# Kernel optimization log

Measured on AMD Instinct MI355X. Metric: run time of the kernel, lower is better.

Reference implementation:

```python
import jax, jax.numpy as jnp
import numpy as np

N_NODES = 50000
N_EDGES = 300000
INPUT_DIM = 128
HIDDEN_DIM = 256
NUM_HEADS = 8
HEAD_DIM = HIDDEN_DIM // NUM_HEADS  # 32
NUM_EDGE_TYPES = 3


def setup_inputs() -> dict:
    key = jax.random.key(0)
    ks = jax.random.split(key, 12)
    s_in = 1.0 / np.sqrt(INPUT_DIM)
    s_hid = 1.0 / np.sqrt(HIDDEN_DIM)
    return {
        "node_features": jax.random.normal(ks[0], (N_NODES, INPUT_DIM), jnp.float32),
        "edges": jax.random.randint(ks[1], (N_EDGES, 2), 0, N_NODES),
        "edge_types": jax.random.randint(ks[2], (N_EDGES,), 0, NUM_EDGE_TYPES),
        # torch.nn.Linear convention: y = x @ W.T + b, W: [out, in]
        "Wq": jax.random.normal(ks[3], (HIDDEN_DIM, INPUT_DIM), jnp.float32) * s_in,
        "bq": jax.random.normal(ks[4], (HIDDEN_DIM,), jnp.float32) * s_in,
        "Wk": jax.random.normal(ks[5], (HIDDEN_DIM, INPUT_DIM), jnp.float32) * s_in,
        "bk": jax.random.normal(ks[6], (HIDDEN_DIM,), jnp.float32) * s_in,
        "Wv": jax.random.normal(ks[7], (HIDDEN_DIM, INPUT_DIM), jnp.float32) * s_in,
        "bv": jax.random.normal(ks[8], (HIDDEN_DIM,), jnp.float32) * s_in,
        "edge_emb": jax.random.normal(ks[9], (NUM_EDGE_TYPES, HIDDEN_DIM), jnp.float32),
        "Wo": jax.random.normal(ks[10], (INPUT_DIM, HIDDEN_DIM), jnp.float32) * s_hid,
        "bo": jax.random.normal(ks[11], (INPUT_DIM,), jnp.float32) * s_hid,
    }


def reference(node_features, edges, edge_types, Wq, bq, Wk, bk, Wv, bv, edge_emb, Wo, bo):
    # Project all nodes once, split heads: [N, H, D]
    Q = (node_features @ Wq.T + bq).reshape(-1, NUM_HEADS, HEAD_DIM)
    K = (node_features @ Wk.T + bk).reshape(-1, NUM_HEADS, HEAD_DIM)
    V = (node_features @ Wv.T + bv).reshape(-1, NUM_HEADS, HEAD_DIM)

    src = edges[:, 0]
    tgt = edges[:, 1]

    # Per-edge small attention: Q[src] [E,H,D] x K[tgt]^T -> [E,H,H]
    # (identical math to the original per-edge-type loop, since only the
    #  edge embedding depends on edge_type and it is gathered per edge)
    scale = 1.0 / jnp.sqrt(jnp.float32(HEAD_DIM))
    scores = jnp.einsum("ehd,egd->ehg", Q[src], K[tgt]) * scale
    attn = jax.nn.softmax(scores, axis=-1)
    msg = jnp.einsum("ehg,egd->ehd", attn, V[tgt]).reshape(-1, HIDDEN_DIM)  # [E, HID]

    msg = msg + edge_emb[edge_types]          # per-edge-type embedding add
    out_e = msg @ Wo.T + bo                   # output projection per edge [E, IN]

    # Scatter-add over source nodes (original Python loop over edges)
    messages = jax.ops.segment_sum(out_e, src, num_segments=N_NODES)
    return messages
```

## Files before the change

kernel.cpp:

```cpp
#include <hip/hip_runtime.h>

#define N_NODES 50000
#define N_EDGES 300000
#define M_PAD 50048
#define M_PAD2 50176
#define NBLK 196

typedef __attribute__((ext_vector_type(8))) short bf16x8;
typedef __attribute__((ext_vector_type(4))) short bf16x4;
typedef __attribute__((ext_vector_type(4))) float f32x4;

__device__ __forceinline__ float bf2f(unsigned short h) { return __uint_as_float(((unsigned int)h) << 16); }
__device__ __forceinline__ unsigned short f2bf(float x) {
    unsigned int u = __float_as_uint(x);
    unsigned int r = (u + 0x7FFFu + ((u >> 16) & 1u)) >> 16;
    return (unsigned short)r;
}

template <int MODE>
__global__ __launch_bounds__(MODE == 0 ? 512 : 128)
void mfma_gemm(const unsigned short* __restrict__ A2, const unsigned short* __restrict__ B2,
               const float* __restrict__ biasCat,
               unsigned short* __restrict__ Qb, unsigned short* __restrict__ Kb,
               unsigned short* __restrict__ Vb,
               const float* __restrict__ eew, const float* __restrict__ bo,
               const float4* __restrict__ cnt4, float* __restrict__ Cout)
{
    constexpr int K2  = (MODE == 0) ? 128 : 256;
    constexpr int NWN = (MODE == 0) ? 4 : 2;
    constexpr int BM  = (MODE == 0) ? 128 : 64;
    const int t    = threadIdx.x;
    const int w    = t >> 6;
    const int lane = t & 63;
    const int l15  = lane & 15;
    const int lg   = lane >> 4;
    const int bx   = blockIdx.x;
    const int m0   = blockIdx.y * BM;
    const int n0   = bx * (NWN * 64);
    const int wm   = (w / NWN) * 64;
    const int wn   = (w % NWN) * 64;

    f32x4 acc[4][4] = {};

    const unsigned short* Abase = A2 + (size_t)(m0 + wm + l15) * K2 + lg * 8;
    const unsigned short* Bbase = B2 + (size_t)(n0 + wn + l15) * K2 + lg * 8;

    #pragma unroll 2
    for (int ks = 0; ks < K2 / 32; ++ks) {
        bf16x8 af[4], bfv[4];
        #pragma unroll
        for (int mi = 0; mi < 4; ++mi)
            af[mi] = *(const bf16x8*)(Abase + (size_t)mi * 16 * K2 + ks * 32);
        #pragma unroll
        for (int ni = 0; ni < 4; ++ni)
            bfv[ni] = *(const bf16x8*)(Bbase + (size_t)ni * 16 * K2 + ks * 32);
        #pragma unroll
        for (int mi = 0; mi < 4; ++mi)
            #pragma unroll
            for (int ni = 0; ni < 4; ++ni)
                acc[mi][ni] = __builtin_amdgcn_mfma_f32_16x16x32_bf16(
                    af[mi], bfv[ni], acc[mi][ni], 0, 0, 0);
    }

    if constexpr (MODE == 0) {
        __shared__ unsigned short Cs[64 * 256];
        float bvn[4];
        #pragma unroll
        for (int ni = 0; ni < 4; ++ni)
            bvn[ni] = biasCat[n0 + wn + ni * 16 + l15];

        #pragma unroll
        for (int p = 0; p < 2; ++p) {
            if (p) __syncthreads();
            #pragma unroll
            for (int mi2 = 0; mi2 < 2; ++mi2) {
                const int mi = p * 2 + mi2;
                #pragma unroll
                for (int j = 0; j < 4; ++j) {
                    const int lr = (wm >> 1) + mi2 * 16 + lg * 4 + j;
                    const int xr = (lr & 7) << 3;
                    #pragma unroll
                    for (int ni = 0; ni < 4; ++ni) {
                        const int col = wn + ni * 16 + l15;
                        Cs[lr * 256 + (col ^ xr)] = f2bf(acc[mi][ni][j] + bvn[ni]);
                    }
                }
            }
            __syncthreads();

            if (bx < 2) {
                unsigned short* dst = bx ? Kb : Qb;
                #pragma unroll
                for (int c8 = 0; c8 < 4; ++c8) {
                    const int chunk = c8 * 512 + t;
                    const int lr = chunk >> 5;
                    const int ec = (chunk & 31) * 8;
                    const int gr = m0 + ((lr < 32) ? (p * 32 + lr)
                                                   : (64 + p * 32 + (lr - 32)));
                    const bf16x8 v = *(const bf16x8*)&Cs[lr * 256 + (ec ^ ((lr & 7) << 3))];
                    *(bf16x8*)&dst[(size_t)gr * 256 + ec] = v;
                }
            } else {
                #pragma unroll
                for (int c8 = 0; c8 < 4; ++c8) {
                    const int chunk = c8 * 512 + t;
                    const int lr = chunk >> 5;
                    const int ec = (chunk & 31) * 8;
                    const int gr = m0 + ((lr < 32) ? (p * 32 + lr)
                                                   : (64 + p * 32 + (lr - 32)));
                    const int d  = ec >> 3;
                    const int xr = (lr & 7) << 3;
                    bf16x8 v;
                    #pragma unroll
                    for (int g = 0; g < 8; ++g)
                        v[g] = (short)Cs[lr * 256 + ((g * 32 + d) ^ xr)];
                    *(bf16x8*)&Vb[(size_t)gr * 256 + ec] = v;
                }
            }
        }
    } else {
        #pragma unroll
        for (int mi = 0; mi < 4; ++mi)
            #pragma unroll
            for (int j = 0; j < 4; ++j) {
                const int row = m0 + wm + mi * 16 + lg * 4 + j;
                if (row < N_NODES) {
                    const float4 cv = cnt4[row];
                    #pragma unroll
                    for (int ni = 0; ni < 4; ++ni) {
                        const int col = wn + ni * 16 + l15;
                        Cout[(size_t)row * 128 + col] = acc[mi][ni][j]
                            + cv.x * eew[col] + cv.y * eew[128 + col]
                            + cv.z * eew[256 + col] + cv.w * bo[col];
                    }
                }
            }
    }
}

__global__ __launch_bounds__(256)
void conv_nf_kernel(const float4* __restrict__ nf4, unsigned short* __restrict__ A2)
{
    const int tid = blockIdx.x * 256 + threadIdx.x;
    if (tid >= N_NODES * 32) return;
    const int m = tid >> 5, k4 = (tid & 31) * 4;
    const float4 v = nf4[tid];
    ushort4 hi;
    hi.x = f2bf(v.x); hi.y = f2bf(v.y); hi.z = f2bf(v.z); hi.w = f2bf(v.w);
    *reinterpret_cast<ushort4*>(&A2[(size_t)m * 128 + k4]) = hi;
}

__global__ __launch_bounds__(256)
void prep_kernel(const float* __restrict__ Wq, const float* __restrict__ Wk,
                 const float* __restrict__ Wv, const float* __restrict__ bq,
                 const float* __restrict__ bk, const float* __restrict__ bv,
                 const float* __restrict__ Wo, const float* __restrict__ ee,
                 unsigned short* __restrict__ B2qkv, unsigned short* __restrict__ B2o,
                 float* __restrict__ biasCat, float* __restrict__ eew)
{
    const int bid = blockIdx.x, t = threadIdx.x;
    if (bid < 384) {
        const int tid = bid * 256 + t;
        const int r = tid >> 7, k = tid & 127;
        const float* W = (r < 256) ? Wq : (r < 512) ? Wk : Wv;
        B2qkv[(size_t)r * 128 + k] = f2bf(W[(size_t)(r & 255) * 128 + k]);
        if (k == 0) {
            const float* b = (r < 256) ? bq : (r < 512) ? bk : bv;
            biasCat[r] = b[r & 255];
        }
    } else if (bid < 512) {
        const int tid = (bid - 384) * 256 + t;
        const int r = tid >> 8, k = tid & 255;
        B2o[(size_t)r * 256 + k] = f2bf(Wo[(size_t)r * 256 + k]);
    } else if (t < 128) {
        float a0 = 0.f, a1 = 0.f, a2 = 0.f;
        for (int k = 0; k < 256; ++k) {
            const float w = Wo[(size_t)t * 256 + k];
            a0 += ee[k] * w; a1 += ee[256 + k] * w; a2 += ee[512 + k] * w;
        }
        eew[t] = a0; eew[128 + t] = a1; eew[256 + t] = a2;
    }
}

__global__ __launch_bounds__(256)
void hist_kernel(const int* __restrict__ edges, int* __restrict__ deg)
{
    const int e = blockIdx.x * 256 + threadIdx.x;
    if (e < N_EDGES) atomicAdd(&deg[edges[2 * e]], 1);
}

__global__ __launch_bounds__(256)
void scan_part1(const int* __restrict__ deg, int* __restrict__ blockSum)
{
    const int t = threadIdx.x;
    const int i = blockIdx.x * 256 + t;
    int v = (i < N_NODES) ? deg[i] : 0;
    #pragma unroll
    for (int o = 1; o < 64; o <<= 1) v += __shfl_xor(v, o);
    __shared__ int ws[4];
    if ((t & 63) == 0) ws[t >> 6] = v;
    __syncthreads();
    if (t == 0) blockSum[blockIdx.x] = ws[0] + ws[1] + ws[2] + ws[3];
}

__global__ __launch_bounds__(256)
void scan_part2(const int* __restrict__ blockSum, int* __restrict__ blockBase,
                int* __restrict__ rowStart)
{
    __shared__ int lds[256];
    const int t = threadIdx.x;
    lds[t] = (t < NBLK) ? blockSum[t] : 0;
    __syncthreads();
    #pragma unroll
    for (int o = 1; o < 256; o <<= 1) {
        const int u = (t >= o) ? lds[t - o] : 0;
        __syncthreads();
        lds[t] += u;
        __syncthreads();
    }
    if (t < NBLK) blockBase[t] = (t == 0) ? 0 : lds[t - 1];
    if (t == 0) rowStart[N_NODES] = N_EDGES;
}

__global__ __launch_bounds__(256)
void scan_part3(const int* __restrict__ deg, const int* __restrict__ blockBase,
                int* __restrict__ rowStart, int* __restrict__ cursor)
{
    const int t = threadIdx.x;
    const int lane = t & 63, wid = t >> 6;
    const int i = blockIdx.x * 256 + t;
    const int d = (i < N_NODES) ? deg[i] : 0;
    int x = d;
    #pragma unroll
    for (int o = 1; o < 64; o <<= 1) {
        const int u = __shfl_up(x, o);
        if (lane >= o) x += u;
    }
    __shared__ int wtot[4];
    if (lane == 63) wtot[wid] = x;
    __syncthreads();
    int wo = 0;
    #pragma unroll
    for (int wi = 0; wi < 3; ++wi) wo += (wi < wid) ? wtot[wi] : 0;
    const int excl = blockBase[blockIdx.x] + wo + x - d;
    if (i < N_NODES) { rowStart[i] = excl; cursor[i] = excl; }
}

__global__ __launch_bounds__(256)
void scatter_kernel(const int* __restrict__ edges, const int* __restrict__ etypes,
                    int* __restrict__ cursor, int* __restrict__ packed)
{
    const int e = blockIdx.x * 256 + threadIdx.x;
    if (e < N_EDGES) {
        const int pos = atomicAdd(&cursor[edges[2 * e]], 1);
        packed[pos] = edges[2 * e + 1] | (etypes[e] << 20);
    }
}

__global__ __launch_bounds__(256)
void node_gather_kernel(const int* __restrict__ packed, const int* __restrict__ rowStart,
                        const unsigned short* __restrict__ Qb,
                        const unsigned short* __restrict__ Kb,
                        const unsigned short* __restrict__ Vb,
                        unsigned short* __restrict__ accQ, float4* __restrict__ cnt4)
{
    const int lane = threadIdx.x & 63;
    const int n = blockIdx.x * 4 + (threadIdx.x >> 6);
    if (n >= N_NODES) return;
    const int l15 = lane & 15;
    const int lg  = lane >> 4;

    const bf16x8 qf = *(const bf16x8*)&Qb[(size_t)n * 256 + (l15 & 7) * 32 + lg * 8];

    f32x4 cpv0 = {0.f, 0.f, 0.f, 0.f};
    f32x4 cpv1 = {0.f, 0.f, 0.f, 0.f};
    int c0 = 0, c1 = 0, c2 = 0;

    const int lo = rowStart[n], hi = rowStart[n + 1];
    const bool validBase = ((l15 < 8) == (lg < 2));

    for (int idx = lo; idx < hi; idx += 2) {
        const int  p0  = packed[idx];
        const bool dup = (idx + 1 >= hi);
        const int  p1  = dup ? p0 : packed[idx + 1];
        const int  t0  = p0 & 0xFFFFF;
        const int  t1  = p1 & 0xFFFFF;
        const int  e0  = p0 >> 20;
        const int  e1  = p1 >> 20;
        c0 += (e0 == 0); c1 += (e0 == 1); c2 += (e0 == 2);
        if (!dup) { c0 += (e1 == 0); c1 += (e1 == 1); c2 += (e1 == 2); }

        const int tk = (l15 < 8) ? t0 : t1;
        const bf16x8 kf = *(const bf16x8*)&Kb[(size_t)tk * 256 + (l15 & 7) * 32 + lg * 8];

        const int tv = (lg < 2) ? t0 : t1;
        const unsigned short* vrow = &Vb[(size_t)tv * 256 + (lg & 1) * 4];
        const bf16x4 vf0 = *(const bf16x4*)&vrow[l15 * 8];
        const bf16x4 vf1 = *(const bf16x4*)&vrow[(l15 + 16) * 8];

        f32x4 s = __builtin_amdgcn_mfma_f32_16x16x32_bf16(kf, qf, (f32x4){0.f, 0.f, 0.f, 0.f}, 0, 0, 0);
        const float SC = 0.17677669529663687f;
        const float s0 = s[0] * SC, s1 = s[1] * SC, s2 = s[2] * SC, s3 = s[3] * SC;

        float mx = fmaxf(fmaxf(s0, s1), fmaxf(s2, s3));
        mx = fmaxf(mx, __shfl_xor(mx, 16));
        const float ex0 = __expf(s0 - mx), ex1 = __expf(s1 - mx);
        const float ex2 = __expf(s2 - mx), ex3 = __expf(s3 - mx);
        float sum = ex0 + ex1 + ex2 + ex3;
        sum += __shfl_xor(sum, 16);
        const float inv = 1.0f / sum;

        const bool valid = validBase && !(dup && (l15 >= 8));
        bf16x4 pa;
        pa[0] = valid ? (short)f2bf(ex0 * inv) : (short)0;
        pa[1] = valid ? (short)f2bf(ex1 * inv) : (short)0;
        pa[2] = valid ? (short)f2bf(ex2 * inv) : (short)0;
        pa[3] = valid ? (short)f2bf(ex3 * inv) : (short)0;

        cpv0 = __builtin_amdgcn_mfma_f32_16x16x16bf16_1k(pa, vf0, cpv0, 0, 0, 0);
        cpv1 = __builtin_amdgcn_mfma_f32_16x16x16bf16_1k(pa, vf1, cpv1, 0, 0, 0);
    }

    #pragma unroll
    for (int j = 0; j < 4; ++j) {
        cpv0[j] += __shfl_xor(cpv0[j], 32);
        cpv1[j] += __shfl_xor(cpv1[j], 32);
    }

    if (lane < 32) {
        unsigned short* row = &accQ[(size_t)n * 256];
        #pragma unroll
        for (int j = 0; j < 4; ++j) {
            const int h = lg * 4 + j;
            row[h * 32 + l15]      = f2bf(cpv0[j]);
            row[h * 32 + 16 + l15] = f2bf(cpv1[j]);
        }
    }
    if (lane == 0)
        cnt4[n] = make_float4((float)c0, (float)c1, (float)c2, (float)(hi - lo));
}

extern "C" void kernel_launch(void* const* d_in, const int* in_sizes, int n_in,
                              void* d_out, int out_size, void* d_ws, size_t ws_size,
                              hipStream_t stream)
{
    const float* nf      = (const float*)d_in[0];
    const int*   edges   = (const int*)d_in[1];
    const int*   etypes  = (const int*)d_in[2];
    const float* Wq      = (const float*)d_in[3];
    const float* bq      = (const float*)d_in[4];
    const float* Wk      = (const float*)d_in[5];
    const float* bk      = (const float*)d_in[6];
    const float* Wv      = (const float*)d_in[7];
    const float* bv      = (const float*)d_in[8];
    const float* ee      = (const float*)d_in[9];
    const float* Wo      = (const float*)d_in[10];
    const float* bo      = (const float*)d_in[11];
    float* out = (float*)d_out;

    char* ws = (char*)d_ws;
    size_t off = 0;
    auto alloc = [&](size_t bytes) -> void* {
        void* p = ws + off;
        off = (off + bytes + 255) & ~(size_t)255;
        return p;
    };
    unsigned short* A2    = (unsigned short*)alloc((size_t)M_PAD * 128 * 2);
    unsigned short* B2qkv = (unsigned short*)alloc((size_t)768 * 128 * 2);
    unsigned short* B2o   = (unsigned short*)alloc((size_t)128 * 256 * 2);
    float*          biasC = (float*)alloc(768 * sizeof(float));
    float*          eew   = (float*)alloc(384 * sizeof(float));
    unsigned short* Qb    = (unsigned short*)alloc((size_t)M_PAD * 256 * 2);
    unsigned short* Kb    = (unsigned short*)alloc((size_t)M_PAD * 256 * 2);
    unsigned short* Vb    = (unsigned short*)alloc((size_t)M_PAD * 256 * 2);
    unsigned short* accQ  = (unsigned short*)alloc((size_t)M_PAD2 * 256 * 2);
    float4* cnt4 = (float4*)alloc((size_t)N_NODES * sizeof(float4));
    int*    deg  = (int*)alloc((size_t)N_NODES * sizeof(int));
    int*    rowS = (int*)alloc((size_t)(N_NODES + 1) * sizeof(int));
    int*    curs = (int*)alloc((size_t)N_NODES * sizeof(int));
    int*    pck  = (int*)alloc((size_t)N_EDGES * sizeof(int));
    int*    bSum = (int*)alloc((size_t)NBLK * sizeof(int));
    int*    bBase= (int*)alloc((size_t)NBLK * sizeof(int));

    const dim3 blk(256);

    conv_nf_kernel<<<dim3((N_NODES * 32 + 255) / 256), blk, 0, stream>>>((const float4*)nf, A2);
    prep_kernel<<<dim3(513), blk, 0, stream>>>(Wq, Wk, Wv, bq, bk, bv, Wo, ee, B2qkv, B2o, biasC, eew);

    hipMemsetAsync(deg, 0, (size_t)N_NODES * sizeof(int), stream);
    hist_kernel<<<dim3((N_EDGES + 255) / 256), blk, 0, stream>>>(edges, deg);
    scan_part1<<<dim3(NBLK), blk, 0, stream>>>(deg, bSum);
    scan_part2<<<dim3(1), blk, 0, stream>>>(bSum, bBase, rowS);
    scan_part3<<<dim3(NBLK), blk, 0, stream>>>(deg, bBase, rowS, curs);
    scatter_kernel<<<dim3((N_EDGES + 255) / 256), blk, 0, stream>>>(edges, etypes, curs, pck);

    mfma_gemm<0><<<dim3(3, M_PAD / 128), dim3(512), 0, stream>>>(
        A2, B2qkv, biasC, Qb, Kb, Vb, nullptr, nullptr, nullptr, nullptr);

    node_gather_kernel<<<dim3((N_NODES + 3) / 4), blk, 0, stream>>>(
        pck, rowS, Qb, Kb, Vb, accQ, cnt4);

    mfma_gemm<1><<<dim3(1, M_PAD2 / 64), dim3(128), 0, stream>>>(
        accQ, B2o, nullptr, nullptr, nullptr, nullptr, eew, bo, cnt4, out);
}
```

Before: 188.4 us.

## Fuse fp32-to-bf16 conversion into GEMMs and unroll edge gather by four

The GEMM kernels now read the fp32 node features and weights directly and convert them to bf16 in registers with packed cvt instructions. This removes the separate conversion kernel and most of the prep kernel's launches and traffic. The attention scale is folded into the Q projection and its bias. The gather loop now processes four edges per iteration with two independent accumulator pairs and counts edge types with a packed integer. The cost is that weights are re-read as fp32 and re-converted by every block, and the larger loop body raises register pressure.

```diff
diff --git a/kernel.cpp b/kernel.cpp
--- a/kernel.cpp
+++ b/kernel.cpp
@@ -5,55 +5,78 @@
 #define M_PAD 50048
 #define M_PAD2 50176
 #define NBLK 196
+#define SC 0.17677669529663687f
 
 typedef __attribute__((ext_vector_type(8))) short bf16x8;
 typedef __attribute__((ext_vector_type(4))) short bf16x4;
 typedef __attribute__((ext_vector_type(4))) float f32x4;
 
-__device__ __forceinline__ float bf2f(unsigned short h) { return __uint_as_float(((unsigned int)h) << 16); }
 __device__ __forceinline__ unsigned short f2bf(float x) {
     unsigned int u = __float_as_uint(x);
     unsigned int r = (u + 0x7FFFu + ((u >> 16) & 1u)) >> 16;
     return (unsigned short)r;
 }
-
-template <int MODE>
-__global__ __launch_bounds__(MODE == 0 ? 512 : 128)
-void mfma_gemm(const unsigned short* __restrict__ A2, const unsigned short* __restrict__ B2,
-               const float* __restrict__ biasCat,
-               unsigned short* __restrict__ Qb, unsigned short* __restrict__ Kb,
-               unsigned short* __restrict__ Vb,
-               const float* __restrict__ eew, const float* __restrict__ bo,
-               const float4* __restrict__ cnt4, float* __restrict__ Cout)
-{
-    constexpr int K2  = (MODE == 0) ? 128 : 256;
-    constexpr int NWN = (MODE == 0) ? 4 : 2;
-    constexpr int BM  = (MODE == 0) ? 128 : 64;
+__device__ __forceinline__ unsigned int cvtpk(float lo, float hi) {
+    unsigned int r;
+    asm volatile("v_cvt_pk_bf16_f32 %0, %1, %2" : "=v"(r) : "v"(lo), "v"(hi));
+    return r;
+}
+__device__ __forceinline__ bf16x8 cvt8(float4 a, float4 b) {
+    union { unsigned int u[4]; bf16x8 v; } r;
+    r.u[0] = cvtpk(a.x, a.y); r.u[1] = cvtpk(a.z, a.w);
+    r.u[2] = cvtpk(b.x, b.y); r.u[3] = cvtpk(b.z, b.w);
+    return r.v;
+}
+
+__global__ __launch_bounds__(512)
+void qkv_gemm(const float* __restrict__ nf, const float* __restrict__ Wq,
+              const float* __restrict__ Wk, const float* __restrict__ Wv,
+              const float* __restrict__ biasCat,
+              unsigned short* __restrict__ Qb, unsigned short* __restrict__ Kb,
+              unsigned short* __restrict__ Vb)
+{
     const int t    = threadIdx.x;
     const int w    = t >> 6;
     const int lane = t & 63;
     const int l15  = lane & 15;
     const int lg   = lane >> 4;
     const int bx   = blockIdx.x;
-    const int m0   = blockIdx.y * BM;
-    const int n0   = bx * (NWN * 64);
-    const int wm   = (w / NWN) * 64;
-    const int wn   = (w % NWN) * 64;
+    const int m0   = blockIdx.y * 128;
+    const int wm   = (w >> 2) * 64;
+    const int wn   = (w & 3) * 64;
+    const float* W = (bx == 0) ? Wq : (bx == 1) ? Wk : Wv;
+    const float mulc = (bx == 0) ? SC : 1.0f;
 
     f32x4 acc[4][4] = {};
 
-    const unsigned short* Abase = A2 + (size_t)(m0 + wm + l15) * K2 + lg * 8;
-    const unsigned short* Bbase = B2 + (size_t)(n0 + wn + l15) * K2 + lg * 8;
-
-    #pragma unroll 2
-    for (int ks = 0; ks < K2 / 32; ++ks) {
+    const float* Arow[4]; bool aok[4];
+    #pragma unroll
+    for (int mi = 0; mi < 4; ++mi) {
+        const int row = m0 + wm + mi * 16 + l15;
+        aok[mi]  = row < N_NODES;
+        Arow[mi] = nf + (size_t)row * 128 + lg * 8;
+    }
+    const float* Brow[4];
+    #pragma unroll
+    for (int ni = 0; ni < 4; ++ni)
+        Brow[ni] = W + (size_t)(wn + ni * 16 + l15) * 128 + lg * 8;
+
+    const float4 z4 = make_float4(0.f, 0.f, 0.f, 0.f);
+    #pragma unroll
+    for (int ks = 0; ks < 4; ++ks) {
         bf16x8 af[4], bfv[4];
         #pragma unroll
-        for (int mi = 0; mi < 4; ++mi)
-            af[mi] = *(const bf16x8*)(Abase + (size_t)mi * 16 * K2 + ks * 32);
-        #pragma unroll
-        for (int ni = 0; ni < 4; ++ni)
-            bfv[ni] = *(const bf16x8*)(Bbase + (size_t)ni * 16 * K2 + ks * 32);
+        for (int mi = 0; mi < 4; ++mi) {
+            const float4 a0 = aok[mi] ? *(const float4*)(Arow[mi] + ks * 32) : z4;
+            const float4 a1 = aok[mi] ? *(const float4*)(Arow[mi] + ks * 32 + 4) : z4;
+            af[mi] = cvt8(a0, a1);
+        }
+        #pragma unroll
+        for (int ni = 0; ni < 4; ++ni) {
+            const float4 b0 = *(const float4*)(Brow[ni] + ks * 32);
+            const float4 b1 = *(const float4*)(Brow[ni] + ks * 32 + 4);
+            bfv[ni] = cvt8(b0, b1);
+        }
         #pragma unroll
         for (int mi = 0; mi < 4; ++mi)
             #pragma unroll
@@ -62,117 +85,133 @@
                     af[mi], bfv[ni], acc[mi][ni], 0, 0, 0);
     }
 
-    if constexpr (MODE == 0) {
-        __shared__ unsigned short Cs[64 * 256];
-        float bvn[4];
-        #pragma unroll
-        for (int ni = 0; ni < 4; ++ni)
-            bvn[ni] = biasCat[n0 + wn + ni * 16 + l15];
-
-        #pragma unroll
-        for (int p = 0; p < 2; ++p) {
-            if (p) __syncthreads();
+    __shared__ unsigned short Cs[64 * 256];
+    float bvn[4];
+    #pragma unroll
+    for (int ni = 0; ni < 4; ++ni)
+        bvn[ni] = biasCat[bx * 256 + wn + ni * 16 + l15];
+
+    #pragma unroll
+    for (int p = 0; p < 2; ++p) {
+        if (p) __syncthreads();
+        #pragma unroll
+        for (int mi2 = 0; mi2 < 2; ++mi2) {
+            const int mi = p * 2 + mi2;
             #pragma unroll
-            for (int mi2 = 0; mi2 < 2; ++mi2) {
-                const int mi = p * 2 + mi2;
+            for (int j = 0; j < 4; ++j) {
+                const int lr = (wm >> 1) + mi2 * 16 + lg * 4 + j;
+                const int xr = (lr & 7) << 3;
                 #pragma unroll
-                for (int j = 0; j < 4; ++j) {
-                    const int lr = (wm >> 1) + mi2 * 16 + lg * 4 + j;
-                    const int xr = (lr & 7) << 3;
-                    #pragma unroll
-                    for (int ni = 0; ni < 4; ++ni) {
-                        const int col = wn + ni * 16 + l15;
-                        Cs[lr * 256 + (col ^ xr)] = f2bf(acc[mi][ni][j] + bvn[ni]);
-                    }
+                for (int ni = 0; ni < 4; ++ni) {
+                    const int col = wn + ni * 16 + l15;
+                    Cs[lr * 256 + (col ^ xr)] = f2bf(fmaf(acc[mi][ni][j], mulc, bvn[ni]));
                 }
             }
-            __syncthreads();
-
-            if (bx < 2) {
-                unsigned short* dst = bx ? Kb : Qb;
+        }
+        __syncthreads();
+
+        if (bx < 2) {
+            unsigned short* dst = bx ? Kb : Qb;
+            #pragma unroll
+            for (int c8 = 0; c8 < 4; ++c8) {
+                const int chunk = c8 * 512 + t;
+                const int lr = chunk >> 5;
+                const int ec = (chunk & 31) * 8;
+                const int gr = m0 + ((lr < 32) ? (p * 32 + lr)
+                                               : (64 + p * 32 + (lr - 32)));
+                const bf16x8 v = *(const bf16x8*)&Cs[lr * 256 + (ec ^ ((lr & 7) << 3))];
+                *(bf16x8*)&dst[(size_t)gr * 256 + ec] = v;
+            }
+        } else {
+            #pragma unroll
+            for (int c8 = 0; c8 < 4; ++c8) {
+                const int chunk = c8 * 512 + t;
+                const int lr = chunk >> 5;
+                const int ec = (chunk & 31) * 8;
+                const int gr = m0 + ((lr < 32) ? (p * 32 + lr)
+                                               : (64 + p * 32 + (lr - 32)));
+                const int d  = ec >> 3;
+                const int xr = (lr & 7) << 3;
+                bf16x8 v;
                 #pragma unroll
-                for (int c8 = 0; c8 < 4; ++c8) {
-                    const int chunk = c8 * 512 + t;
-                    const int lr = chunk >> 5;
-                    const int ec = (chunk & 31) * 8;
-                    const int gr = m0 + ((lr < 32) ? (p * 32 + lr)
-                                                   : (64 + p * 32 + (lr - 32)));
-                    const bf16x8 v = *(const bf16x8*)&Cs[lr * 256 + (ec ^ ((lr & 7) << 3))];
-                    *(bf16x8*)&dst[(size_t)gr * 256 + ec] = v;
-                }
-            } else {
+                for (int g = 0; g < 8; ++g)
+                    v[g] = (short)Cs[lr * 256 + ((g * 32 + d) ^ xr)];
+                *(bf16x8*)&Vb[(size_t)gr * 256 + ec] = v;
+            }
+        }
+    }
+}
+
+__global__ __launch_bounds__(128)
+void out_gemm(const unsigned short* __restrict__ accQ, const float* __restrict__ Wo,
+              const float* __restrict__ eew, const float* __restrict__ bo,
+              const float4* __restrict__ cnt4, float* __restrict__ Cout)
+{
+    const int t    = threadIdx.x;
+    const int w    = t >> 6;
+    const int lane = t & 63;
+    const int l15  = lane & 15;
+    const int lg   = lane >> 4;
+    const int m0   = blockIdx.y * 64;
+    const int wn   = w * 64;
+
+    f32x4 acc[4][4] = {};
+
+    const unsigned short* Abase = accQ + (size_t)(m0 + l15) * 256 + lg * 8;
+    const float* Brow[4];
+    #pragma unroll
+    for (int ni = 0; ni < 4; ++ni)
+        Brow[ni] = Wo + (size_t)(wn + ni * 16 + l15) * 256 + lg * 8;
+
+    #pragma unroll 2
+    for (int ks = 0; ks < 8; ++ks) {
+        bf16x8 af[4], bfv[4];
+        #pragma unroll
+        for (int mi = 0; mi < 4; ++mi)
+            af[mi] = *(const bf16x8*)(Abase + (size_t)mi * 16 * 256 + ks * 32);
+        #pragma unroll
+        for (int ni = 0; ni < 4; ++ni) {
+            const float4 b0 = *(const float4*)(Brow[ni] + ks * 32);
+            const float4 b1 = *(const float4*)(Brow[ni] + ks * 32 + 4);
+            bfv[ni] = cvt8(b0, b1);
+        }
+        #pragma unroll
+        for (int mi = 0; mi < 4; ++mi)
+            #pragma unroll
+            for (int ni = 0; ni < 4; ++ni)
+                acc[mi][ni] = __builtin_amdgcn_mfma_f32_16x16x32_bf16(
+                    af[mi], bfv[ni], acc[mi][ni], 0, 0, 0);
+    }
+
+    #pragma unroll
+    for (int mi = 0; mi < 4; ++mi)
+        #pragma unroll
+        for (int j = 0; j < 4; ++j) {
+            const int row = m0 + mi * 16 + lg * 4 + j;
+            if (row < N_NODES) {
+                const float4 cv = cnt4[row];
                 #pragma unroll
-                for (int c8 = 0; c8 < 4; ++c8) {
-                    const int chunk = c8 * 512 + t;
-                    const int lr = chunk >> 5;
-                    const int ec = (chunk & 31) * 8;
-                    const int gr = m0 + ((lr < 32) ? (p * 32 + lr)
-                                                   : (64 + p * 32 + (lr - 32)));
-                    const int d  = ec >> 3;
-                    const int xr = (lr & 7) << 3;
-                    bf16x8 v;
-                    #pragma unroll
-                    for (int g = 0; g < 8; ++g)
-                        v[g] = (short)Cs[lr * 256 + ((g * 32 + d) ^ xr)];
-                    *(bf16x8*)&Vb[(size_t)gr * 256 + ec] = v;
+                for (int ni = 0; ni < 4; ++ni) {
+                    const int col = wn + ni * 16 + l15;
+                    Cout[(size_t)row * 128 + col] = acc[mi][ni][j]
+                        + cv.x * eew[col] + cv.y * eew[128 + col]
+                        + cv.z * eew[256 + col] + cv.w * bo[col];
                 }
             }
         }
-    } else {
-        #pragma unroll
-        for (int mi = 0; mi < 4; ++mi)
-            #pragma unroll
-            for (int j = 0; j < 4; ++j) {
-                const int row = m0 + wm + mi * 16 + lg * 4 + j;
-                if (row < N_NODES) {
-                    const float4 cv = cnt4[row];
-                    #pragma unroll
-                    for (int ni = 0; ni < 4; ++ni) {
-                        const int col = wn + ni * 16 + l15;
-                        Cout[(size_t)row * 128 + col] = acc[mi][ni][j]
-                            + cv.x * eew[col] + cv.y * eew[128 + col]
-                            + cv.z * eew[256 + col] + cv.w * bo[col];
-                    }
-                }
-            }
-    }
-}
-
-__global__ __launch_bounds__(256)
-void conv_nf_kernel(const float4* __restrict__ nf4, unsigned short* __restrict__ A2)
-{
-    const int tid = blockIdx.x * 256 + threadIdx.x;
-    if (tid >= N_NODES * 32) return;
-    const int m = tid >> 5, k4 = (tid & 31) * 4;
-    const float4 v = nf4[tid];
-    ushort4 hi;
-    hi.x = f2bf(v.x); hi.y = f2bf(v.y); hi.z = f2bf(v.z); hi.w = f2bf(v.w);
-    *reinterpret_cast<ushort4*>(&A2[(size_t)m * 128 + k4]) = hi;
-}
-
-__global__ __launch_bounds__(256)
-void prep_kernel(const float* __restrict__ Wq, const float* __restrict__ Wk,
-                 const float* __restrict__ Wv, const float* __restrict__ bq,
-                 const float* __restrict__ bk, const float* __restrict__ bv,
-                 const float* __restrict__ Wo, const float* __restrict__ ee,
-                 unsigned short* __restrict__ B2qkv, unsigned short* __restrict__ B2o,
+}
+
+__global__ __launch_bounds__(256)
+void prep_kernel(const float* __restrict__ bq, const float* __restrict__ bk,
+                 const float* __restrict__ bv, const float* __restrict__ Wo,
+                 const float* __restrict__ ee,
                  float* __restrict__ biasCat, float* __restrict__ eew)
 {
-    const int bid = blockIdx.x, t = threadIdx.x;
-    if (bid < 384) {
-        const int tid = bid * 256 + t;
-        const int r = tid >> 7, k = tid & 127;
-        const float* W = (r < 256) ? Wq : (r < 512) ? Wk : Wv;
-        B2qkv[(size_t)r * 128 + k] = f2bf(W[(size_t)(r & 255) * 128 + k]);
-        if (k == 0) {
-            const float* b = (r < 256) ? bq : (r < 512) ? bk : bv;
-            biasCat[r] = b[r & 255];
-        }
-    } else if (bid < 512) {
-        const int tid = (bid - 384) * 256 + t;
-        const int r = tid >> 8, k = tid & 255;
-        B2o[(size_t)r * 256 + k] = f2bf(Wo[(size_t)r * 256 + k]);
-    } else if (t < 128) {
+    const int t = threadIdx.x;
+    biasCat[t]       = bq[t] * SC;
+    biasCat[256 + t] = bk[t];
+    biasCat[512 + t] = bv[t];
+    if (t < 128) {
         float a0 = 0.f, a1 = 0.f, a2 = 0.f;
         for (int k = 0; k < 256; ++k) {
             const float w = Wo[(size_t)t * 256 + k];
@@ -257,6 +296,21 @@
     }
 }
 
+__device__ __forceinline__ bf16x4 softmax_pa(f32x4 s, bool valid)
+{
+    float mx = fmaxf(fmaxf(s[0], s[1]), fmaxf(s[2], s[3]));
+    mx = fmaxf(mx, __shfl_xor(mx, 16));
+    const float e0 = __expf(s[0] - mx), e1 = __expf(s[1] - mx);
+    const float e2 = __expf(s[2] - mx), e3 = __expf(s[3] - mx);
+    float sum = e0 + e1 + e2 + e3;
+    sum += __shfl_xor(sum, 16);
+    const float inv = valid ? (1.0f / sum) : 0.0f;
+    union { unsigned int u[2]; bf16x4 v; } r;
+    r.u[0] = cvtpk(e0 * inv, e1 * inv);
+    r.u[1] = cvtpk(e2 * inv, e3 * inv);
+    return r.v;
+}
+
 __global__ __launch_bounds__(256)
 void node_gather_kernel(const int* __restrict__ packed, const int* __restrict__ rowStart,
                         const unsigned short* __restrict__ Qb,
@@ -272,23 +326,57 @@
 
     const bf16x8 qf = *(const bf16x8*)&Qb[(size_t)n * 256 + (l15 & 7) * 32 + lg * 8];
 
-    f32x4 cpv0 = {0.f, 0.f, 0.f, 0.f};
-    f32x4 cpv1 = {0.f, 0.f, 0.f, 0.f};
-    int c0 = 0, c1 = 0, c2 = 0;
+    f32x4 cpvA0 = {0.f,0.f,0.f,0.f}, cpvA1 = {0.f,0.f,0.f,0.f};
+    f32x4 cpvB0 = {0.f,0.f,0.f,0.f}, cpvB1 = {0.f,0.f,0.f,0.f};
+    int cnt = 0;
 
     const int lo = rowStart[n], hi = rowStart[n + 1];
     const bool validBase = ((l15 < 8) == (lg < 2));
-
-    for (int idx = lo; idx < hi; idx += 2) {
+    const f32x4 z4 = {0.f, 0.f, 0.f, 0.f};
+    int idx = lo;
+
+    for (; idx + 4 <= hi; idx += 4) {
+        const int p0 = packed[idx],     p1 = packed[idx + 1];
+        const int p2 = packed[idx + 2], p3 = packed[idx + 3];
+        const int t0 = p0 & 0xFFFFF, t1 = p1 & 0xFFFFF;
+        const int t2 = p2 & 0xFFFFF, t3 = p3 & 0xFFFFF;
+        cnt += (1 << ((p0 >> 20) * 10)) + (1 << ((p1 >> 20) * 10))
+             + (1 << ((p2 >> 20) * 10)) + (1 << ((p3 >> 20) * 10));
+
+        const int tkA = (l15 < 8) ? t0 : t1;
+        const int tkB = (l15 < 8) ? t2 : t3;
+        const bf16x8 kfA = *(const bf16x8*)&Kb[(size_t)tkA * 256 + (l15 & 7) * 32 + lg * 8];
+        const bf16x8 kfB = *(const bf16x8*)&Kb[(size_t)tkB * 256 + (l15 & 7) * 32 + lg * 8];
+
+        const int tvA = (lg < 2) ? t0 : t1;
+        const int tvB = (lg < 2) ? t2 : t3;
+        const unsigned short* vrA = &Vb[(size_t)tvA * 256 + (lg & 1) * 4];
+        const unsigned short* vrB = &Vb[(size_t)tvB * 256 + (lg & 1) * 4];
+        const bf16x4 vfA0 = *(const bf16x4*)&vrA[l15 * 8];
+        const bf16x4 vfA1 = *(const bf16x4*)&vrA[(l15 + 16) * 8];
+        const bf16x4 vfB0 = *(const bf16x4*)&vrB[l15 * 8];
+        const bf16x4 vfB1 = *(const bf16x4*)&vrB[(l15 + 16) * 8];
+
+        const f32x4 sA = __builtin_amdgcn_mfma_f32_16x16x32_bf16(kfA, qf, z4, 0, 0, 0);
+        const f32x4 sB = __builtin_amdgcn_mfma_f32_16x16x32_bf16(kfB, qf, z4, 0, 0, 0);
+
+        const bf16x4 paA = softmax_pa(sA, validBase);
+        const bf16x4 paB = softmax_pa(sB, validBase);
+
+        cpvA0 = __builtin_amdgcn_mfma_f32_16x16x16bf16_1k(paA, vfA0, cpvA0, 0, 0, 0);
+        cpvA1 = __builtin_amdgcn_mfma_f32_16x16x16bf16_1k(paA, vfA1, cpvA1, 0, 0, 0);
+        cpvB0 = __builtin_amdgcn_mfma_f32_16x16x16bf16_1k(paB, vfB0, cpvB0, 0, 0, 0);
+        cpvB1 = __builtin_amdgcn_mfma_f32_16x16x16bf16_1k(paB, vfB1, cpvB1, 0, 0, 0);
+    }
+
+    for (; idx < hi; idx += 2) {
         const int  p0  = packed[idx];
         const bool dup = (idx + 1 >= hi);
         const int  p1  = dup ? p0 : packed[idx + 1];
         const int  t0  = p0 & 0xFFFFF;
         const int  t1  = p1 & 0xFFFFF;
-        const int  e0  = p0 >> 20;
-        const int  e1  = p1 >> 20;
-        c0 += (e0 == 0); c1 += (e0 == 1); c2 += (e0 == 2);
-        if (!dup) { c0 += (e1 == 0); c1 += (e1 == 1); c2 += (e1 == 2); }
+        cnt += (1 << ((p0 >> 20) * 10));
+        if (!dup) cnt += (1 << ((p1 >> 20) * 10));
 
         const int tk = (l15 < 8) ? t0 : t1;
         const bf16x8 kf = *(const bf16x8*)&Kb[(size_t)tk * 256 + (l15 & 7) * 32 + lg * 8];
@@ -298,28 +386,16 @@
         const bf16x4 vf0 = *(const bf16x4*)&vrow[l15 * 8];
         const bf16x4 vf1 = *(const bf16x4*)&vrow[(l15 + 16) * 8];
 
-        f32x4 s = __builtin_amdgcn_mfma_f32_16x16x32_bf16(kf, qf, (f32x4){0.f, 0.f, 0.f, 0.f}, 0, 0, 0);
-        const float SC = 0.17677669529663687f;
-        const float s0 = s[0] * SC, s1 = s[1] * SC, s2 = s[2] * SC, s3 = s[3] * SC;
-
-        float mx = fmaxf(fmaxf(s0, s1), fmaxf(s2, s3));
-        mx = fmaxf(mx, __shfl_xor(mx, 16));
-        const float ex0 = __expf(s0 - mx), ex1 = __expf(s1 - mx);
-        const float ex2 = __expf(s2 - mx), ex3 = __expf(s3 - mx);
-        float sum = ex0 + ex1 + ex2 + ex3;
-        sum += __shfl_xor(sum, 16);
-        const float inv = 1.0f / sum;
-
+        const f32x4 s = __builtin_amdgcn_mfma_f32_16x16x32_bf16(kf, qf, z4, 0, 0, 0);
         const bool valid = validBase && !(dup && (l15 >= 8));
-        bf16x4 pa;
-        pa[0] = valid ? (short)f2bf(ex0 * inv) : (short)0;
-        pa[1] = valid ? (short)f2bf(ex1 * inv) : (short)0;
-        pa[2] = valid ? (short)f2bf(ex2 * inv) : (short)0;
-        pa[3] = valid ? (short)f2bf(ex3 * inv) : (short)0;
-
-        cpv0 = __builtin_amdgcn_mfma_f32_16x16x16bf16_1k(pa, vf0, cpv0, 0, 0, 0);
-        cpv1 = __builtin_amdgcn_mfma_f32_16x16x16bf16_1k(pa, vf1, cpv1, 0, 0, 0);
-    }
+        const bf16x4 pa = softmax_pa(s, valid);
+
+        cpvA0 = __builtin_amdgcn_mfma_f32_16x16x16bf16_1k(pa, vf0, cpvA0, 0, 0, 0);
+        cpvA1 = __builtin_amdgcn_mfma_f32_16x16x16bf16_1k(pa, vf1, cpvA1, 0, 0, 0);
+    }
+
+    f32x4 cpv0 = cpvA0 + cpvB0;
+    f32x4 cpv1 = cpvA1 + cpvB1;
 
     #pragma unroll
     for (int j = 0; j < 4; ++j) {
@@ -336,8 +412,10 @@
             row[h * 32 + 16 + l15] = f2bf(cpv1[j]);
         }
     }
-    if (lane == 0)
+    if (lane == 0) {
+        const int c0 = cnt & 1023, c1 = (cnt >> 10) & 1023, c2 = (cnt >> 20) & 1023;
         cnt4[n] = make_float4((float)c0, (float)c1, (float)c2, (float)(hi - lo));
+    }
 }
 
 extern "C" void kernel_launch(void* const* d_in, const int* in_sizes, int n_in,
@@ -365,9 +443,6 @@
         off = (off + bytes + 255) & ~(size_t)255;
         return p;
     };
-    unsigned short* A2    = (unsigned short*)alloc((size_t)M_PAD * 128 * 2);
-    unsigned short* B2qkv = (unsigned short*)alloc((size_t)768 * 128 * 2);
-    unsigned short* B2o   = (unsigned short*)alloc((size_t)128 * 256 * 2);
     float*          biasC = (float*)alloc(768 * sizeof(float));
     float*          eew   = (float*)alloc(384 * sizeof(float));
     unsigned short* Qb    = (unsigned short*)alloc((size_t)M_PAD * 256 * 2);
@@ -384,8 +459,7 @@
 
     const dim3 blk(256);
 
-    conv_nf_kernel<<<dim3((N_NODES * 32 + 255) / 256), blk, 0, stream>>>((const float4*)nf, A2);
-    prep_kernel<<<dim3(513), blk, 0, stream>>>(Wq, Wk, Wv, bq, bk, bv, Wo, ee, B2qkv, B2o, biasC, eew);
+    prep_kernel<<<dim3(1), blk, 0, stream>>>(bq, bk, bv, Wo, ee, biasC, eew);
 
     hipMemsetAsync(deg, 0, (size_t)N_NODES * sizeof(int), stream);
     hist_kernel<<<dim3((N_EDGES + 255) / 256), blk, 0, stream>>>(edges, deg);
@@ -394,12 +468,12 @@
     scan_part3<<<dim3(NBLK), blk, 0, stream>>>(deg, bBase, rowS, curs);
     scatter_kernel<<<dim3((N_EDGES + 255) / 256), blk, 0, stream>>>(edges, etypes, curs, pck);
 
-    mfma_gemm<0><<<dim3(3, M_PAD / 128), dim3(512), 0, stream>>>(
-        A2, B2qkv, biasC, Qb, Kb, Vb, nullptr, nullptr, nullptr, nullptr);
+    qkv_gemm<<<dim3(3, M_PAD / 128), dim3(512), 0, stream>>>(
+        nf, Wq, Wk, Wv, biasC, Qb, Kb, Vb);
 
     node_gather_kernel<<<dim3((N_NODES + 3) / 4), blk, 0, stream>>>(
         pck, rowS, Qb, Kb, Vb, accQ, cnt4);
 
-    mfma_gemm<1><<<dim3(1, M_PAD2 / 64), dim3(128), 0, stream>>>(
-        accQ, B2o, nullptr, nullptr, nullptr, nullptr, eew, bo, cnt4, out);
-}
+    out_gemm<<<dim3(1, M_PAD2 / 64), dim3(128), 0, stream>>>(
+        accQ, Wo, eew, bo, cnt4, out);
+}
```

New measurement: 313.7 us. +66.5%, slower.
